# Kernel tuning notes

Hardware: AMD Instinct MI355X
Metric: run time of the kernel (lower is better)

The kernel has to match this reference:

```python
import jax, jax.numpy as jnp
import numpy as np

L, V, P, D, H, F = 6, 50257, 1024, 1024, 16, 4096
DH = D // H
EPS = 1e-5


def setup_inputs() -> dict:
    key = jax.random.key(0)
    ks = jax.random.split(key, 8)
    s = 0.02  # init scale to keep activations sane across layers
    inp = {
        "input_ids": jax.random.randint(ks[0], (2, 1024), 0, V),
        "wte": jax.random.normal(ks[1], (V, D), jnp.float32) * s,
        "wpe": jax.random.normal(ks[2], (P, D), jnp.float32) * s,
        "ln1_g": jnp.ones((L, D), jnp.float32),
        "ln1_b": jnp.zeros((L, D), jnp.float32),
        "wq": jax.random.normal(ks[3], (L, D, D), jnp.float32) * s,
        "bq": jnp.zeros((L, D), jnp.float32),
        "wk": jax.random.normal(ks[4], (L, D, D), jnp.float32) * s,
        "bk": jnp.zeros((L, D), jnp.float32),
        "wv": jax.random.normal(ks[5], (L, D, D), jnp.float32) * s,
        "bv": jnp.zeros((L, D), jnp.float32),
        "wo": jax.random.normal(jax.random.fold_in(key, 10), (L, D, D), jnp.float32) * s,
        "bo": jnp.zeros((L, D), jnp.float32),
        "ln2_g": jnp.ones((L, D), jnp.float32),
        "ln2_b": jnp.zeros((L, D), jnp.float32),
        "w1": jax.random.normal(ks[6], (L, D, F), jnp.float32) * s,
        "b1": jnp.zeros((L, F), jnp.float32),
        "w2": jax.random.normal(ks[7], (L, F, D), jnp.float32) * s,
        "b2": jnp.zeros((L, D), jnp.float32),
        "lnf_g": jnp.ones((D,), jnp.float32),
        "lnf_b": jnp.zeros((D,), jnp.float32),
    }
    return inp


def _ln(x, g, b):
    m = jnp.mean(x, axis=-1, keepdims=True)
    v = jnp.mean(jnp.square(x - m), axis=-1, keepdims=True)
    return (x - m) * jax.lax.rsqrt(v + EPS) * g + b


def _block(x, p):
    (g1, be1, wq, bq, wk, bk, wv, bv, wo, bo, g2, be2, w1, b1, w2, b2) = p
    B, T, _ = x.shape
    h = _ln(x, g1, be1)
    q = (h @ wq + bq).reshape(B, T, H, DH)
    k = (h @ wk + bk).reshape(B, T, H, DH)
    v = (h @ wv + bv).reshape(B, T, H, DH)
    scores = jnp.einsum("bqhd,bkhd->bhqk", q, k) * (1.0 / np.sqrt(DH))
    attn = jax.nn.softmax(scores, axis=-1)  # NOTE: no causal mask (as in source)
    o = jnp.einsum("bhqk,bkhd->bqhd", attn, v).reshape(B, T, D)
    x = x + o @ wo + bo
    h2 = _ln(x, g2, be2)
    x = x + jax.nn.gelu(h2 @ w1 + b1, approximate=False) @ w2 + b2
    return x


def reference(input_ids, wte, wpe, ln1_g, ln1_b, wq, bq, wk, bk, wv, bv,
              wo, bo, ln2_g, ln2_b, w1, b1, w2, b2, lnf_g, lnf_b):
    T = input_ids.shape[1]
    x = wte[input_ids] + wpe[:T]  # [B,T,D]
    params = (ln1_g, ln1_b, wq, bq, wk, bk, wv, bv, wo, bo,
              ln2_g, ln2_b, w1, b1, w2, b2)

    def step(x, p):
        return _block(x, p), None

    x, _ = jax.lax.scan(step, x, params)
    return _ln(x, lnf_g, lnf_b)
```

## Files before the change

### kernel.cpp

```cpp
#include <hip/hip_runtime.h>
#include <hip/hip_bf16.h>
#include <math.h>

#define DV 1024
#define FF 4096
#define NLAY 6
#define NH 16
#define TT 1024
#define NTOK 2048

typedef float f32x4 __attribute__((ext_vector_type(4)));
typedef short bf16x8 __attribute__((ext_vector_type(8)));
typedef unsigned short u16;
typedef u16 u16x4 __attribute__((ext_vector_type(4)));
typedef u16 u16x8 __attribute__((ext_vector_type(8)));

__device__ __forceinline__ u16 f2b(float f) {
  unsigned u = __float_as_uint(f);
  unsigned r = (u + 0x7fffu + ((u >> 16) & 1u)) >> 16;
  return (u16)r;
}
__device__ __forceinline__ float b2f(u16 u) {
  return __uint_as_float(((unsigned)u) << 16);
}

__device__ __forceinline__ void gload_lds16(const void* g, void* lds) {
  __builtin_amdgcn_global_load_lds(
      (const __attribute__((address_space(1))) void*)g,
      (__attribute__((address_space(3))) void*)lds, 16, 0, 0);
}

__global__ __launch_bounds__(256) void embed_ln_k(const int* __restrict__ ids,
                                                  const float* __restrict__ wte,
                                                  const float* __restrict__ wpe,
                                                  const float* __restrict__ gg,
                                                  const float* __restrict__ bb,
                                                  float* __restrict__ X,
                                                  u16* __restrict__ outb) {
  int row = blockIdx.x, tid = threadIdx.x;
  int t = row & (TT - 1);
  int id = ids[row];
  f32x4 a = *(const f32x4*)(wte + (size_t)id * DV + tid * 4);
  f32x4 p = *(const f32x4*)(wpe + (size_t)t * DV + tid * 4);
  f32x4 v = a + p;
  *(f32x4*)(X + (size_t)row * DV + tid * 4) = v;
  float s1 = v[0] + v[1] + v[2] + v[3];
  float s2 = v[0] * v[0] + v[1] * v[1] + v[2] * v[2] + v[3] * v[3];
#pragma unroll
  for (int o = 32; o >= 1; o >>= 1) {
    s1 += __shfl_xor(s1, o);
    s2 += __shfl_xor(s2, o);
  }
  __shared__ float sh[8];
  int w = tid >> 6;
  if ((tid & 63) == 0) { sh[w] = s1; sh[w + 4] = s2; }
  __syncthreads();
  s1 = sh[0] + sh[1] + sh[2] + sh[3];
  s2 = sh[4] + sh[5] + sh[6] + sh[7];
  float mean = s1 * (1.0f / DV);
  float var = s2 * (1.0f / DV) - mean * mean;
  float rstd = rsqrtf(var + 1e-5f);
  f32x4 gv = *(const f32x4*)(gg + tid * 4);
  f32x4 bv = *(const f32x4*)(bb + tid * 4);
  u16x4 r;
#pragma unroll
  for (int i = 0; i < 4; ++i) r[i] = f2b((v[i] - mean) * rstd * gv[i] + bv[i]);
  *(u16x4*)(outb + (size_t)row * DV + tid * 4) = r;
}

template <int OUTF>
__global__ __launch_bounds__(256) void ln_k(const float* __restrict__ X,
                                            const float* __restrict__ gg,
                                            const float* __restrict__ bb,
                                            u16* __restrict__ outb,
                                            float* __restrict__ outf) {
  int row = blockIdx.x, tid = threadIdx.x;
  f32x4 v = *(const f32x4*)(X + (size_t)row * DV + tid * 4);
  float s1 = v[0] + v[1] + v[2] + v[3];
  float s2 = v[0] * v[0] + v[1] * v[1] + v[2] * v[2] + v[3] * v[3];
#pragma unroll
  for (int o = 32; o >= 1; o >>= 1) {
    s1 += __shfl_xor(s1, o);
    s2 += __shfl_xor(s2, o);
  }
  __shared__ float sh[8];
  int w = tid >> 6;
  if ((tid & 63) == 0) { sh[w] = s1; sh[w + 4] = s2; }
  __syncthreads();
  s1 = sh[0] + sh[1] + sh[2] + sh[3];
  s2 = sh[4] + sh[5] + sh[6] + sh[7];
  float mean = s1 * (1.0f / DV);
  float var = s2 * (1.0f / DV) - mean * mean;
  float rstd = rsqrtf(var + 1e-5f);
  f32x4 gv = *(const f32x4*)(gg + tid * 4);
  f32x4 bv = *(const f32x4*)(bb + tid * 4);
  f32x4 o;
#pragma unroll
  for (int i = 0; i < 4; ++i) o[i] = (v[i] - mean) * rstd * gv[i] + bv[i];
  if (OUTF) {
    *(f32x4*)(outf + (size_t)row * DV + tid * 4) = o;
  } else {
    u16x4 r = {f2b(o[0]), f2b(o[1]), f2b(o[2]), f2b(o[3])};
    *(u16x4*)(outb + (size_t)row * DV + tid * 4) = r;
  }
}

template <int NS, int OUTF>
__global__ __launch_bounds__(256) void reduce_ln_k(
    float* __restrict__ X, const u16* __restrict__ pp,
    const float* __restrict__ bias, const float* __restrict__ gg,
    const float* __restrict__ bb, u16* __restrict__ outb,
    float* __restrict__ outf) {
  int row = blockIdx.x, tid = threadIdx.x;
  size_t off = (size_t)row * DV + tid * 4;
  f32x4 v = *(const f32x4*)(X + off);
  if (NS > 0) {
    f32x4 bvv = *(const f32x4*)(bias + tid * 4);
    v += bvv;
#pragma unroll
    for (int s = 0; s < NS; ++s) {
      u16x4 pv = *(const u16x4*)(pp + (size_t)s * NTOK * DV + off);
      v[0] += b2f(pv[0]); v[1] += b2f(pv[1]);
      v[2] += b2f(pv[2]); v[3] += b2f(pv[3]);
    }
    *(f32x4*)(X + off) = v;
  }
  float s1 = v[0] + v[1] + v[2] + v[3];
  float s2 = v[0] * v[0] + v[1] * v[1] + v[2] * v[2] + v[3] * v[3];
#pragma unroll
  for (int o = 32; o >= 1; o >>= 1) {
    s1 += __shfl_xor(s1, o);
    s2 += __shfl_xor(s2, o);
  }
  __shared__ float sh[8];
  int w = tid >> 6;
  if ((tid & 63) == 0) { sh[w] = s1; sh[w + 4] = s2; }
  __syncthreads();
  s1 = sh[0] + sh[1] + sh[2] + sh[3];
  s2 = sh[4] + sh[5] + sh[6] + sh[7];
  float mean = s1 * (1.0f / DV);
  float var = s2 * (1.0f / DV) - mean * mean;
  float rstd = rsqrtf(var + 1e-5f);
  f32x4 gv = *(const f32x4*)(gg + tid * 4);
  f32x4 bv = *(const f32x4*)(bb + tid * 4);
  f32x4 o;
#pragma unroll
  for (int i = 0; i < 4; ++i) o[i] = (v[i] - mean) * rstd * gv[i] + bv[i];
  if (OUTF) {
    *(f32x4*)(outf + off) = o;
  } else {
    u16x4 r = {f2b(o[0]), f2b(o[1]), f2b(o[2]), f2b(o[3])};
    *(u16x4*)(outb + off) = r;
  }
}

__global__ __launch_bounds__(256) void transw_k(const float* __restrict__ wq,
                                                const float* __restrict__ wk,
                                                const float* __restrict__ wv,
                                                const float* __restrict__ wo,
                                                const float* __restrict__ w1,
                                                const float* __restrict__ w2,
                                                u16* __restrict__ WT) {
  int lay = blockIdx.y;
  size_t oDD = (size_t)lay * DV * DV, oDF = (size_t)lay * DV * FF;
  u16* WTL = WT + (size_t)lay * 12 * 1024 * 1024;
  int bid = blockIdx.x;
  const float* src;
  u16* dst;
  int K, N, tile;
  if (bid < 256) {
    int which = bid >> 6;
    src = (which == 0 ? wq : which == 1 ? wk : which == 2 ? wv : wo) + oDD;
    dst = WTL + (size_t)which * (DV * DV);
    K = DV; N = DV; tile = bid & 63;
  } else if (bid < 512) {
    src = w1 + oDF; dst = WTL + (size_t)4 * (DV * DV); K = DV; N = FF; tile = bid - 256;
  } else {
    src = w2 + oDF; dst = WTL + (size_t)8 * (DV * DV); K = FF; N = DV; tile = bid - 512;
  }
  int ntc = N >> 7;
  int tr = tile / ntc, tc = tile - tr * ntc;
  int k0 = tr * 128, n0 = tc * 128;
  __shared__ u16 ts[128][130];
  int tid = threadIdx.x;
  int lr = tid >> 5, lc = (tid & 31) * 4;
#pragma unroll
  for (int p = 0; p < 16; ++p) {
    int k = p * 8 + lr;
    f32x4 v = *(const f32x4*)(src + (size_t)(k0 + k) * N + n0 + lc);
    ts[k][lc + 0] = f2b(v[0]);
    ts[k][lc + 1] = f2b(v[1]);
    ts[k][lc + 2] = f2b(v[2]);
    ts[k][lc + 3] = f2b(v[3]);
  }
  __syncthreads();
  int m = tid & 15, wn2 = tid >> 4;
#pragma unroll
  for (int p = 0; p < 8; ++p) {
    int n = p * 16 + wn2;
#pragma unroll
    for (int p2 = 0; p2 < 2; ++p2) {
      int kk = p2 * 64 + m * 4;
      u16x4 ov = {ts[kk][n], ts[kk + 1][n], ts[kk + 2][n], ts[kk + 3][n]};
      *(u16x4*)(dst + (size_t)(n0 + n) * K + k0 + kk) = ov;
    }
  }
}

template <int EPI>
__global__ __launch_bounds__(256) void gemm_k(
    const u16* __restrict__ A, const u16* __restrict__ Wt,
    const float* __restrict__ b0, const float* __restrict__ b1,
    const float* __restrict__ b2, u16* __restrict__ o0, u16* __restrict__ o1,
    u16* __restrict__ o2t, u16* __restrict__ op, float* __restrict__ of,
    const float* __restrict__ res, int M, int N, int K, int KS) {
  int z = blockIdx.z;
  const u16* W = Wt;
  const float* bias = b0;
  u16* outb = o0;
  if (EPI == 0) {
    W = Wt + (size_t)z * N * K;
    bias = z == 0 ? b0 : z == 1 ? b1 : b2;
    outb = z == 0 ? o0 : o1;
  }
  int kbeg = (EPI == 3) ? z * KS : 0;
  int klen = (EPI == 3) ? KS : K;
  int bm = blockIdx.x * 128, bn = blockIdx.y * 128;
  __shared__ __attribute__((aligned(16))) u16 As[2][128 * 64];
  __shared__ __attribute__((aligned(16))) u16 Bs[2][128 * 64];
  int tid = threadIdx.x, l = tid & 63, w = tid >> 6;
  int q = l & 15, g = l >> 4;
  int wm = (w >> 1) * 64, wn = (w & 1) * 64;
  int srow = w * 32 + (l >> 3);
  int scol = (((l & 7) ^ ((l >> 3) & 7))) * 8;
  const u16* Ab = A + (size_t)(bm + srow) * K + kbeg + scol;
  const u16* Wb = W + (size_t)(bn + srow) * K + kbeg + scol;
  f32x4 acc[4][4] = {};
  int nk = klen >> 6;
#pragma unroll
  for (int i = 0; i < 4; ++i) {
    gload_lds16(Ab + (size_t)i * 8 * K, &As[0][(w * 32 + i * 8) * 64]);
    gload_lds16(Wb + (size_t)i * 8 * K, &Bs[0][(w * 32 + i * 8) * 64]);
  }
  __syncthreads();
  for (int t = 0; t < nk; ++t) {
    int cur = t & 1;
    if (t + 1 < nk) {
      int ko = (t + 1) * 64;
#pragma unroll
      for (int i = 0; i < 4; ++i) {
        gload_lds16(Ab + (size_t)i * 8 * K + ko, &As[cur ^ 1][(w * 32 + i * 8) * 64]);
        gload_lds16(Wb + (size_t)i * 8 * K + ko, &Bs[cur ^ 1][(w * 32 + i * 8) * 64]);
      }
    }
#pragma unroll
    for (int kk = 0; kk < 2; ++kk) {
      bf16x8 af[4], bfr[4];
#pragma unroll
      for (int f = 0; f < 4; ++f) {
        int ra = wm + f * 16 + q, rb = wn + f * 16 + q;
        af[f]  = *(const bf16x8*)(&As[cur][ra * 64 + ((kk * 4 + g) ^ (ra & 7)) * 8]);
        bfr[f] = *(const bf16x8*)(&Bs[cur][rb * 64 + ((kk * 4 + g) ^ (rb & 7)) * 8]);
      }
#pragma unroll
      for (int fm = 0; fm < 4; ++fm)
#pragma unroll
        for (int fn = 0; fn < 4; ++fn)
          acc[fm][fn] = __builtin_amdgcn_mfma_f32_16x16x32_bf16(af[fm], bfr[fn],
                                                                acc[fm][fn], 0, 0, 0);
    }
    __syncthreads();
  }
#pragma unroll
  for (int fm = 0; fm < 4; ++fm) {
#pragma unroll
    for (int fn = 0; fn < 4; ++fn) {
      int gcol = bn + wn + fn * 16 + q;
      int growb = bm + wm + fm * 16 + g * 4;
      if (EPI == 3) {
        u16* pf = op + (size_t)z * M * N;
#pragma unroll
        for (int r = 0; r < 4; ++r)
          pf[(size_t)(growb + r) * N + gcol] = f2b(acc[fm][fn][r]);
      } else if (EPI == 0 && z == 2) {
        float bv = bias[gcol];
        u16x4 pv = {f2b(acc[fm][fn][0] + bv), f2b(acc[fm][fn][1] + bv),
                    f2b(acc[fm][fn][2] + bv), f2b(acc[fm][fn][3] + bv)};
        *(u16x4*)(o2t + (size_t)gcol * M + growb) = pv;
      } else {
        float bv = bias[gcol];
#pragma unroll
        for (int r = 0; r < 4; ++r) {
          float v = acc[fm][fn][r] + bv;
          if (EPI == 1) v = 0.5f * v * (1.0f + erff(v * 0.70710678118f));
          if (EPI == 2) {
            of[(size_t)(growb + r) * N + gcol] = res[(size_t)(growb + r) * N + gcol] + v;
          } else {
            outb[(size_t)(growb + r) * N + gcol] = f2b(v);
          }
        }
      }
    }
  }
}

__global__ __launch_bounds__(256) void attn_k(const u16* __restrict__ Q,
                                              const u16* __restrict__ Kb,
                                              const u16* __restrict__ Vt,
                                              u16* __restrict__ O) {
  int bid = blockIdx.x;
  int qt = bid & 15, h = (bid >> 4) & 15, b = bid >> 8;
  int tid = threadIdx.x, l = tid & 63, w = tid >> 6;
  int q = l & 15, g = l >> 4;
  int tokbase = b * TT;
  int qbase = tokbase + qt * 64 + w * 16;
  __shared__ __attribute__((aligned(16))) u16 Ks[2][32 * 64];
  __shared__ __attribute__((aligned(16))) u16 Vs[2][64 * 32];
  __shared__ __attribute__((aligned(16))) u16 Ps[4][512];
  bf16x8 qf[2];
  {
    int qrow = qbase + q;
#pragma unroll
    for (int half = 0; half < 2; ++half)
      qf[half] = *(const bf16x8*)(Q + (size_t)qrow * DV + h * 64 + half * 32 + g * 8);
  }
  int key_s = w * 8 + (l >> 3), c_s = l & 7;
  const u16* ksrc = Kb + (size_t)(tokbase + key_s) * DV + h * 64 + ((c_s ^ (key_s & 7)) * 8);
  int dl = w * 16 + (l >> 2), c2 = l & 3;
  const u16* vsrc = Vt + (size_t)(h * 64 + dl) * NTOK + tokbase + ((c2 ^ (dl & 3)) * 8);
  f32x4 oacc[4] = {};
  float m_run = -INFINITY, l_run = 0.0f;
  gload_lds16(ksrc, &Ks[0][w * 512]);
  gload_lds16(vsrc, &Vs[0][w * 512]);
  __syncthreads();
  for (int kbk = 0; kbk < TT / 32; ++kbk) {
    int cur = kbk & 1;
    if (kbk + 1 < TT / 32) {
      gload_lds16(ksrc + (size_t)(kbk + 1) * 32 * DV, &Ks[cur ^ 1][w * 512]);
      gload_lds16(vsrc + (kbk + 1) * 32, &Vs[cur ^ 1][w * 512]);
    }
    f32x4 s[2] = {};
#pragma unroll
    for (int kt = 0; kt < 2; ++kt)
#pragma unroll
      for (int half = 0; half < 2; ++half) {
        int row = kt * 16 + q;
        int chunk = (half * 4 + g) ^ (row & 7);
        bf16x8 kf = *(const bf16x8*)(&Ks[cur][row * 64 + chunk * 8]);
        s[kt] = __builtin_amdgcn_mfma_f32_16x16x32_bf16(kf, qf[half], s[kt], 0, 0, 0);
      }
    float tmax = -INFINITY;
#pragma unroll
    for (int kt = 0; kt < 2; ++kt)
#pragma unroll
      for (int r = 0; r < 4; ++r) {
        s[kt][r] *= 0.125f;
        tmax = fmaxf(tmax, s[kt][r]);
      }
    tmax = fmaxf(tmax, __shfl_xor(tmax, 16));
    tmax = fmaxf(tmax, __shfl_xor(tmax, 32));
    float m_new = fmaxf(m_run, tmax);
    float corr = __expf(m_run - m_new);
    float psum = 0.0f;
    u16 pb[2][4];
#pragma unroll
    for (int kt = 0; kt < 2; ++kt)
#pragma unroll
      for (int r = 0; r < 4; ++r) {
        float p = __expf(s[kt][r] - m_new);
        psum += p;
        pb[kt][r] = f2b(p);
      }
    psum += __shfl_xor(psum, 16);
    psum += __shfl_xor(psum, 32);
    l_run = l_run * corr + psum;
    m_run = m_new;
#pragma unroll
    for (int kt = 0; kt < 2; ++kt) {
      u16x4 pv4 = {pb[kt][0], pb[kt][1], pb[kt][2], pb[kt][3]};
      *(u16x4*)(&Ps[w][q * 32 + ((kt * 4 + g) ^ (q & 7)) * 4]) = pv4;
    }
    float corr4[4];
#pragma unroll
    for (int r = 0; r < 4; ++r) corr4[r] = __shfl(corr, g * 4 + r);
#pragma unroll
    for (int nt = 0; nt < 4; ++nt)
#pragma unroll
      for (int r = 0; r < 4; ++r) oacc[nt][r] *= corr4[r];
    u16x4 a0 = *(const u16x4*)(&Ps[w][q * 32 + ((2 * g) ^ (q & 7)) * 4]);
    u16x4 a1 = *(const u16x4*)(&Ps[w][q * 32 + ((2 * g + 1) ^ (q & 7)) * 4]);
    bf16x8 pa = {(short)a0[0], (short)a0[1], (short)a0[2], (short)a0[3],
                 (short)a1[0], (short)a1[1], (short)a1[2], (short)a1[3]};
#pragma unroll
    for (int nt = 0; nt < 4; ++nt) {
      int vrow = nt * 16 + q;
      int vc = g ^ (vrow & 3);
      bf16x8 vf = *(const bf16x8*)(&Vs[cur][vrow * 32 + vc * 8]);
      oacc[nt] = __builtin_amdgcn_mfma_f32_16x16x32_bf16(pa, vf, oacc[nt], 0, 0, 0);
    }
    __syncthreads();
  }
  float rl[4];
#pragma unroll
  for (int r = 0; r < 4; ++r) rl[r] = 1.0f / __shfl(l_run, g * 4 + r);
#pragma unroll
  for (int nt = 0; nt < 4; ++nt)
#pragma unroll
    for (int r = 0; r < 4; ++r) {
      int qrw = qbase + g * 4 + r;
      int d = nt * 16 + q;
      O[(size_t)qrw * DV + h * 64 + d] = f2b(oacc[nt][r] * rl[r]);
    }
}

extern "C" void kernel_launch(void* const* d_in, const int* in_sizes, int n_in,
                              void* d_out, int out_size, void* d_ws, size_t ws_size,
                              hipStream_t stream) {
  const int*   ids = (const int*)d_in[0];
  const float* wte = (const float*)d_in[1];
  const float* wpe = (const float*)d_in[2];
  const float* l1g = (const float*)d_in[3];
  const float* l1b = (const float*)d_in[4];
  const float* wq  = (const float*)d_in[5];
  const float* bq  = (const float*)d_in[6];
  const float* wk  = (const float*)d_in[7];
  const float* bk  = (const float*)d_in[8];
  const float* wv  = (const float*)d_in[9];
  const float* bv  = (const float*)d_in[10];
  const float* wo  = (const float*)d_in[11];
  const float* bo  = (const float*)d_in[12];
  const float* l2g = (const float*)d_in[13];
  const float* l2b = (const float*)d_in[14];
  const float* w1  = (const float*)d_in[15];
  const float* b1  = (const float*)d_in[16];
  const float* w2  = (const float*)d_in[17];
  const float* b2  = (const float*)d_in[18];
  const float* lfg = (const float*)d_in[19];
  const float* lfb = (const float*)d_in[20];
  (void)in_sizes; (void)n_in; (void)out_size;

  bool bigws = ws_size >= ((size_t)221 << 20);
  bool midws = ws_size >= ((size_t)101 << 20);

  char* ws = (char*)d_ws;
  float* x   = (float*)(ws + 0);
  u16*   hb  = (u16*)(ws + ((size_t)8 << 20));
  u16*   qb  = (u16*)(ws + ((size_t)12 << 20));
  u16*   kb  = (u16*)(ws + ((size_t)16 << 20));
  u16*   vbt = (u16*)(ws + ((size_t)20 << 20));
  u16*   ab  = (u16*)(ws + ((size_t)24 << 20));
  u16*   mb  = (u16*)(ws + ((size_t)28 << 20));
  u16*   pp  = (u16*)(ws + ((size_t)44 << 20));
  u16*   WT  = (u16*)(ws + ((size_t)(midws ? 76 : 44) << 20));

  if (bigws)
    transw_k<<<dim3(768, 6), 256, 0, stream>>>(wq, wk, wv, wo, w1, w2, WT);
  embed_ln_k<<<NTOK, 256, 0, stream>>>(ids, wte, wpe, l1g, l1b, x, hb);

  for (int lay = 0; lay < NLAY; ++lay) {
    size_t oDD = (size_t)lay * DV * DV;
    size_t oDF = (size_t)lay * DV * FF;
    u16* WTL = bigws ? WT + (size_t)lay * 12 * 1024 * 1024 : WT;
    if (!bigws)
      transw_k<<<dim3(768, 1), 256, 0, stream>>>(wq + oDD, wk + oDD, wv + oDD,
                                                 wo + oDD, w1 + oDF, w2 + oDF, WTL);
    gemm_k<0><<<dim3(16, 8, 3), 256, 0, stream>>>(
        hb, WTL, bq + lay * DV, bk + lay * DV, bv + lay * DV,
        qb, kb, vbt, nullptr, nullptr, nullptr, NTOK, DV, DV, 0);
    attn_k<<<512, 256, 0, stream>>>(qb, kb, vbt, ab);
    if (midws) {
      gemm_k<3><<<dim3(16, 8, 4), 256, 0, stream>>>(
          ab, WTL + (size_t)3 * DV * DV, nullptr, nullptr, nullptr,
          nullptr, nullptr, nullptr, pp, nullptr, nullptr, NTOK, DV, DV, 256);
      reduce_ln_k<4, 0><<<NTOK, 256, 0, stream>>>(
          x, pp, bo + lay * DV, l2g + lay * DV, l2b + lay * DV, hb, nullptr);
    } else {
      gemm_k<2><<<dim3(16, 8, 1), 256, 0, stream>>>(
          ab, WTL + (size_t)3 * DV * DV, bo + lay * DV, nullptr, nullptr,
          nullptr, nullptr, nullptr, nullptr, x, x, NTOK, DV, DV, 0);
      ln_k<0><<<NTOK, 256, 0, stream>>>(x, l2g + lay * DV, l2b + lay * DV, hb, nullptr);
    }
    gemm_k<1><<<dim3(16, 32, 1), 256, 0, stream>>>(
        hb, WTL + (size_t)4 * DV * DV, b1 + lay * FF, nullptr, nullptr,
        mb, nullptr, nullptr, nullptr, nullptr, nullptr, NTOK, FF, DV, 0);
    if (midws) {
      gemm_k<3><<<dim3(16, 8, 4), 256, 0, stream>>>(
          mb, WTL + (size_t)8 * DV * DV, nullptr, nullptr, nullptr,
          nullptr, nullptr, nullptr, pp, nullptr, nullptr, NTOK, DV, FF, 1024);
      if (lay < NLAY - 1)
        reduce_ln_k<4, 0><<<NTOK, 256, 0, stream>>>(
            x, pp, b2 + lay * DV, l1g + (lay + 1) * DV, l1b + (lay + 1) * DV,
            hb, nullptr);
      else
        reduce_ln_k<4, 1><<<NTOK, 256, 0, stream>>>(
            x, pp, b2 + lay * DV, lfg, lfb, nullptr, (float*)d_out);
    } else {
      gemm_k<2><<<dim3(16, 8, 1), 256, 0, stream>>>(
          mb, WTL + (size_t)8 * DV * DV, b2 + lay * DV, nullptr, nullptr,
          nullptr, nullptr, nullptr, nullptr, x, x, NTOK, DV, FF, 0);
      if (lay < NLAY - 1)
        ln_k<0><<<NTOK, 256, 0, stream>>>(x, l1g + (lay + 1) * DV,
                                          l1b + (lay + 1) * DV, hb, nullptr);
      else
        ln_k<1><<<NTOK, 256, 0, stream>>>(x, lfg, lfb, nullptr, (float*)d_out);
    }
  }
}
```

Measured before the change: 996.0 us.

## Triple-buffer GEMM K-loop with BK=32 and vmcnt-based waits

```diff
diff --git a/kernel.cpp b/kernel.cpp
--- a/kernel.cpp
+++ b/kernel.cpp
@@ -184,14 +184,17 @@
   __shared__ u16 ts[128][130];
   int tid = threadIdx.x;
   int lr = tid >> 5, lc = (tid & 31) * 4;
+  f32x4 vv[16];
+#pragma unroll
+  for (int p = 0; p < 16; ++p)
+    vv[p] = *(const f32x4*)(src + (size_t)(k0 + p * 8 + lr) * N + n0 + lc);
 #pragma unroll
   for (int p = 0; p < 16; ++p) {
     int k = p * 8 + lr;
-    f32x4 v = *(const f32x4*)(src + (size_t)(k0 + k) * N + n0 + lc);
-    ts[k][lc + 0] = f2b(v[0]);
-    ts[k][lc + 1] = f2b(v[1]);
-    ts[k][lc + 2] = f2b(v[2]);
-    ts[k][lc + 3] = f2b(v[3]);
+    ts[k][lc + 0] = f2b(vv[p][0]);
+    ts[k][lc + 1] = f2b(vv[p][1]);
+    ts[k][lc + 2] = f2b(vv[p][2]);
+    ts[k][lc + 3] = f2b(vv[p][3]);
   }
   __syncthreads();
   int m = tid & 15, wn2 = tid >> 4;
@@ -226,51 +229,54 @@
   int kbeg = (EPI == 3) ? z * KS : 0;
   int klen = (EPI == 3) ? KS : K;
   int bm = blockIdx.x * 128, bn = blockIdx.y * 128;
-  __shared__ __attribute__((aligned(16))) u16 As[2][128 * 64];
-  __shared__ __attribute__((aligned(16))) u16 Bs[2][128 * 64];
+  __shared__ __attribute__((aligned(16))) u16 As[3][128 * 32];
+  __shared__ __attribute__((aligned(16))) u16 Bs[3][128 * 32];
   int tid = threadIdx.x, l = tid & 63, w = tid >> 6;
   int q = l & 15, g = l >> 4;
   int wm = (w >> 1) * 64, wn = (w & 1) * 64;
-  int srow = w * 32 + (l >> 3);
-  int scol = (((l & 7) ^ ((l >> 3) & 7))) * 8;
-  const u16* Ab = A + (size_t)(bm + srow) * K + kbeg + scol;
-  const u16* Wb = W + (size_t)(bn + srow) * K + kbeg + scol;
+  const u16* Asrc = A + (size_t)(bm + (tid >> 2)) * K + kbeg + (tid & 3) * 8;
+  const u16* Wsrc = W + (size_t)(bn + (tid >> 2)) * K + kbeg + (tid & 3) * 8;
+  size_t rstep = (size_t)64 * K;
   f32x4 acc[4][4] = {};
-  int nk = klen >> 6;
-#pragma unroll
-  for (int i = 0; i < 4; ++i) {
-    gload_lds16(Ab + (size_t)i * 8 * K, &As[0][(w * 32 + i * 8) * 64]);
-    gload_lds16(Wb + (size_t)i * 8 * K, &Bs[0][(w * 32 + i * 8) * 64]);
-  }
-  __syncthreads();
+  int nk = klen >> 5;
+#define STG(b, t)                                              \
+  {                                                            \
+    int ko = (t) * 32;                                         \
+    gload_lds16(Asrc + ko, &As[b][tid * 8]);                   \
+    gload_lds16(Asrc + rstep + ko, &As[b][(tid + 256) * 8]);   \
+    gload_lds16(Wsrc + ko, &Bs[b][tid * 8]);                   \
+    gload_lds16(Wsrc + rstep + ko, &Bs[b][(tid + 256) * 8]);   \
+  }
+  STG(0, 0);
+  STG(1, 1);
   for (int t = 0; t < nk; ++t) {
-    int cur = t & 1;
-    if (t + 1 < nk) {
-      int ko = (t + 1) * 64;
-#pragma unroll
-      for (int i = 0; i < 4; ++i) {
-        gload_lds16(Ab + (size_t)i * 8 * K + ko, &As[cur ^ 1][(w * 32 + i * 8) * 64]);
-        gload_lds16(Wb + (size_t)i * 8 * K + ko, &Bs[cur ^ 1][(w * 32 + i * 8) * 64]);
-      }
-    }
-#pragma unroll
-    for (int kk = 0; kk < 2; ++kk) {
-      bf16x8 af[4], bfr[4];
-#pragma unroll
-      for (int f = 0; f < 4; ++f) {
-        int ra = wm + f * 16 + q, rb = wn + f * 16 + q;
-        af[f]  = *(const bf16x8*)(&As[cur][ra * 64 + ((kk * 4 + g) ^ (ra & 7)) * 8]);
-        bfr[f] = *(const bf16x8*)(&Bs[cur][rb * 64 + ((kk * 4 + g) ^ (rb & 7)) * 8]);
-      }
-#pragma unroll
-      for (int fm = 0; fm < 4; ++fm)
-#pragma unroll
-        for (int fn = 0; fn < 4; ++fn)
-          acc[fm][fn] = __builtin_amdgcn_mfma_f32_16x16x32_bf16(af[fm], bfr[fn],
-                                                                acc[fm][fn], 0, 0, 0);
-    }
-    __syncthreads();
-  }
+    __builtin_amdgcn_sched_barrier(0);
+    if (t + 2 < nk) {
+      asm volatile("s_waitcnt vmcnt(4)" ::: "memory");
+    } else {
+      asm volatile("s_waitcnt vmcnt(0)" ::: "memory");
+    }
+    __builtin_amdgcn_s_barrier();
+    __builtin_amdgcn_sched_barrier(0);
+    if (t + 2 < nk) {
+      int b2i = (t + 2) % 3;
+      STG(b2i, t + 2);
+    }
+    int cur = t % 3;
+    bf16x8 af[4], bfr[4];
+#pragma unroll
+    for (int f = 0; f < 4; ++f) {
+      af[f]  = *(const bf16x8*)(&As[cur][(wm + f * 16 + q) * 32 + g * 8]);
+      bfr[f] = *(const bf16x8*)(&Bs[cur][(wn + f * 16 + q) * 32 + g * 8]);
+    }
+#pragma unroll
+    for (int fm = 0; fm < 4; ++fm)
+#pragma unroll
+      for (int fn = 0; fn < 4; ++fn)
+        acc[fm][fn] = __builtin_amdgcn_mfma_f32_16x16x32_bf16(af[fm], bfr[fn],
+                                                              acc[fm][fn], 0, 0, 0);
+  }
+#undef STG
 #pragma unroll
   for (int fm = 0; fm < 4; ++fm) {
 #pragma unroll
```

Measured after the change: 1.109 ms. 11.3% more time.

## Stage GEMM epilogue through LDS for vectorized stores; split V projection; retune split-K

Applied to the files above, without the earlier changes.

```diff
diff --git a/kernel.cpp b/kernel.cpp
--- a/kernel.cpp
+++ b/kernel.cpp
@@ -164,7 +164,8 @@
   int lay = blockIdx.y;
   size_t oDD = (size_t)lay * DV * DV, oDF = (size_t)lay * DV * FF;
   u16* WTL = WT + (size_t)lay * 12 * 1024 * 1024;
-  int bid = blockIdx.x;
+  int b0 = blockIdx.x;
+  int bid = (b0 & 7) * 96 + (b0 >> 3);
   const float* src;
   u16* dst;
   int K, N, tile;
@@ -184,23 +185,26 @@
   __shared__ u16 ts[128][130];
   int tid = threadIdx.x;
   int lr = tid >> 5, lc = (tid & 31) * 4;
+  f32x4 vv[16];
+#pragma unroll
+  for (int p = 0; p < 16; ++p)
+    vv[p] = *(const f32x4*)(src + (size_t)(k0 + p * 8 + lr) * N + n0 + lc);
 #pragma unroll
   for (int p = 0; p < 16; ++p) {
     int k = p * 8 + lr;
-    f32x4 v = *(const f32x4*)(src + (size_t)(k0 + k) * N + n0 + lc);
-    ts[k][lc + 0] = f2b(v[0]);
-    ts[k][lc + 1] = f2b(v[1]);
-    ts[k][lc + 2] = f2b(v[2]);
-    ts[k][lc + 3] = f2b(v[3]);
-  }
-  __syncthreads();
-  int m = tid & 15, wn2 = tid >> 4;
+    ts[k][lc + 0] = f2b(vv[p][0]);
+    ts[k][lc + 1] = f2b(vv[p][1]);
+    ts[k][lc + 2] = f2b(vv[p][2]);
+    ts[k][lc + 3] = f2b(vv[p][3]);
+  }
+  __syncthreads();
+  int m = tid & 15, u2 = tid >> 4;
 #pragma unroll
   for (int p = 0; p < 8; ++p) {
-    int n = p * 16 + wn2;
-#pragma unroll
-    for (int p2 = 0; p2 < 2; ++p2) {
-      int kk = p2 * 64 + m * 4;
+    int n = p * 16 + u2;
+#pragma unroll
+    for (int s = 0; s < 2; ++s) {
+      int kk = s * 64 + m * 4;
       u16x4 ov = {ts[kk][n], ts[kk + 1][n], ts[kk + 2][n], ts[kk + 3][n]};
       *(u16x4*)(dst + (size_t)(n0 + n) * K + k0 + kk) = ov;
     }
@@ -211,7 +215,7 @@
 __global__ __launch_bounds__(256) void gemm_k(
     const u16* __restrict__ A, const u16* __restrict__ Wt,
     const float* __restrict__ b0, const float* __restrict__ b1,
-    const float* __restrict__ b2, u16* __restrict__ o0, u16* __restrict__ o1,
+    u16* __restrict__ o0, u16* __restrict__ o1,
     u16* __restrict__ o2t, u16* __restrict__ op, float* __restrict__ of,
     const float* __restrict__ res, int M, int N, int K, int KS) {
   int z = blockIdx.z;
@@ -220,14 +224,16 @@
   u16* outb = o0;
   if (EPI == 0) {
     W = Wt + (size_t)z * N * K;
-    bias = z == 0 ? b0 : z == 1 ? b1 : b2;
+    bias = z == 0 ? b0 : b1;
     outb = z == 0 ? o0 : o1;
   }
   int kbeg = (EPI == 3) ? z * KS : 0;
   int klen = (EPI == 3) ? KS : K;
   int bm = blockIdx.x * 128, bn = blockIdx.y * 128;
-  __shared__ __attribute__((aligned(16))) u16 As[2][128 * 64];
-  __shared__ __attribute__((aligned(16))) u16 Bs[2][128 * 64];
+  __shared__ __attribute__((aligned(16))) u16 SM[32768];
+  u16* As = SM;
+  u16* Bs = SM + 16384;
+  u16* Cs = SM;
   int tid = threadIdx.x, l = tid & 63, w = tid >> 6;
   int q = l & 15, g = l >> 4;
   int wm = (w >> 1) * 64, wn = (w & 1) * 64;
@@ -239,8 +245,8 @@
   int nk = klen >> 6;
 #pragma unroll
   for (int i = 0; i < 4; ++i) {
-    gload_lds16(Ab + (size_t)i * 8 * K, &As[0][(w * 32 + i * 8) * 64]);
-    gload_lds16(Wb + (size_t)i * 8 * K, &Bs[0][(w * 32 + i * 8) * 64]);
+    gload_lds16(Ab + (size_t)i * 8 * K, &As[(w * 32 + i * 8) * 64]);
+    gload_lds16(Wb + (size_t)i * 8 * K, &Bs[(w * 32 + i * 8) * 64]);
   }
   __syncthreads();
   for (int t = 0; t < nk; ++t) {
@@ -249,8 +255,10 @@
       int ko = (t + 1) * 64;
 #pragma unroll
       for (int i = 0; i < 4; ++i) {
-        gload_lds16(Ab + (size_t)i * 8 * K + ko, &As[cur ^ 1][(w * 32 + i * 8) * 64]);
-        gload_lds16(Wb + (size_t)i * 8 * K + ko, &Bs[cur ^ 1][(w * 32 + i * 8) * 64]);
+        gload_lds16(Ab + (size_t)i * 8 * K + ko,
+                    &As[(cur ^ 1) * 8192 + (w * 32 + i * 8) * 64]);
+        gload_lds16(Wb + (size_t)i * 8 * K + ko,
+                    &Bs[(cur ^ 1) * 8192 + (w * 32 + i * 8) * 64]);
       }
     }
 #pragma unroll
@@ -259,8 +267,8 @@
 #pragma unroll
       for (int f = 0; f < 4; ++f) {
         int ra = wm + f * 16 + q, rb = wn + f * 16 + q;
-        af[f]  = *(const bf16x8*)(&As[cur][ra * 64 + ((kk * 4 + g) ^ (ra & 7)) * 8]);
-        bfr[f] = *(const bf16x8*)(&Bs[cur][rb * 64 + ((kk * 4 + g) ^ (rb & 7)) * 8]);
+        af[f]  = *(const bf16x8*)(&As[cur * 8192 + ra * 64 + ((kk * 4 + g) ^ (ra & 7)) * 8]);
+        bfr[f] = *(const bf16x8*)(&Bs[cur * 8192 + rb * 64 + ((kk * 4 + g) ^ (rb & 7)) * 8]);
       }
 #pragma unroll
       for (int fm = 0; fm < 4; ++fm)
@@ -271,34 +279,52 @@
     }
     __syncthreads();
   }
+  if (EPI == 2) {
+#pragma unroll
+    for (int fm = 0; fm < 4; ++fm)
+#pragma unroll
+      for (int fn = 0; fn < 4; ++fn) {
+        int gcol = bn + wn + fn * 16 + q;
+        int growb = bm + wm + fm * 16 + g * 4;
+        float bv = bias[gcol];
+#pragma unroll
+        for (int r = 0; r < 4; ++r)
+          of[(size_t)(growb + r) * N + gcol] = res[(size_t)(growb + r) * N + gcol]
+                                               + acc[fm][fn][r] + bv;
+      }
+    return;
+  }
 #pragma unroll
   for (int fm = 0; fm < 4; ++fm) {
 #pragma unroll
     for (int fn = 0; fn < 4; ++fn) {
-      int gcol = bn + wn + fn * 16 + q;
-      int growb = bm + wm + fm * 16 + g * 4;
-      if (EPI == 3) {
-        u16* pf = op + (size_t)z * M * N;
-#pragma unroll
-        for (int r = 0; r < 4; ++r)
-          pf[(size_t)(growb + r) * N + gcol] = f2b(acc[fm][fn][r]);
-      } else if (EPI == 0 && z == 2) {
-        float bv = bias[gcol];
-        u16x4 pv = {f2b(acc[fm][fn][0] + bv), f2b(acc[fm][fn][1] + bv),
-                    f2b(acc[fm][fn][2] + bv), f2b(acc[fm][fn][3] + bv)};
-        *(u16x4*)(o2t + (size_t)gcol * M + growb) = pv;
+      int cL = wn + fn * 16 + q;
+      float bv = (EPI == 3) ? 0.0f : bias[bn + cL];
+#pragma unroll
+      for (int r = 0; r < 4; ++r) {
+        int rL = wm + fm * 16 + g * 4 + r;
+        float v = acc[fm][fn][r] + bv;
+        if (EPI == 1) v = 0.5f * v * (1.0f + erff(v * 0.70710678118f));
+        if (EPI == 4) Cs[cL * 132 + rL] = f2b(v);
+        else          Cs[rL * 132 + cL] = f2b(v);
+      }
+    }
+  }
+  __syncthreads();
+  {
+    int rowL = tid >> 4, c8 = (tid & 15) * 8;
+#pragma unroll
+    for (int p = 0; p < 8; ++p) {
+      int row = p * 16 + rowL;
+      u16x4 lo = *(const u16x4*)(&Cs[row * 132 + c8]);
+      u16x4 hi = *(const u16x4*)(&Cs[row * 132 + c8 + 4]);
+      u16x8 ov = {lo[0], lo[1], lo[2], lo[3], hi[0], hi[1], hi[2], hi[3]};
+      if (EPI == 4) {
+        *(u16x8*)(o2t + (size_t)(bn + row) * M + bm + c8) = ov;
+      } else if (EPI == 3) {
+        *(u16x8*)(op + (size_t)z * M * N + (size_t)(bm + row) * N + bn + c8) = ov;
       } else {
-        float bv = bias[gcol];
-#pragma unroll
-        for (int r = 0; r < 4; ++r) {
-          float v = acc[fm][fn][r] + bv;
-          if (EPI == 1) v = 0.5f * v * (1.0f + erff(v * 0.70710678118f));
-          if (EPI == 2) {
-            of[(size_t)(growb + r) * N + gcol] = res[(size_t)(growb + r) * N + gcol] + v;
-          } else {
-            outb[(size_t)(growb + r) * N + gcol] = f2b(v);
-          }
-        }
+        *(u16x8*)(outb + (size_t)(bm + row) * N + bn + c8) = ov;
       }
     }
   }
@@ -464,28 +490,31 @@
     if (!bigws)
       transw_k<<<dim3(768, 1), 256, 0, stream>>>(wq + oDD, wk + oDD, wv + oDD,
                                                  wo + oDD, w1 + oDF, w2 + oDF, WTL);
-    gemm_k<0><<<dim3(16, 8, 3), 256, 0, stream>>>(
-        hb, WTL, bq + lay * DV, bk + lay * DV, bv + lay * DV,
-        qb, kb, vbt, nullptr, nullptr, nullptr, NTOK, DV, DV, 0);
+    gemm_k<0><<<dim3(16, 8, 2), 256, 0, stream>>>(
+        hb, WTL, bq + lay * DV, bk + lay * DV,
+        qb, kb, nullptr, nullptr, nullptr, nullptr, NTOK, DV, DV, 0);
+    gemm_k<4><<<dim3(16, 8, 1), 256, 0, stream>>>(
+        hb, WTL + (size_t)2 * DV * DV, bv + lay * DV, nullptr,
+        nullptr, nullptr, vbt, nullptr, nullptr, nullptr, NTOK, DV, DV, 0);
     attn_k<<<512, 256, 0, stream>>>(qb, kb, vbt, ab);
     if (midws) {
-      gemm_k<3><<<dim3(16, 8, 4), 256, 0, stream>>>(
-          ab, WTL + (size_t)3 * DV * DV, nullptr, nullptr, nullptr,
-          nullptr, nullptr, nullptr, pp, nullptr, nullptr, NTOK, DV, DV, 256);
-      reduce_ln_k<4, 0><<<NTOK, 256, 0, stream>>>(
+      gemm_k<3><<<dim3(16, 8, 2), 256, 0, stream>>>(
+          ab, WTL + (size_t)3 * DV * DV, nullptr, nullptr,
+          nullptr, nullptr, nullptr, pp, nullptr, nullptr, NTOK, DV, DV, 512);
+      reduce_ln_k<2, 0><<<NTOK, 256, 0, stream>>>(
           x, pp, bo + lay * DV, l2g + lay * DV, l2b + lay * DV, hb, nullptr);
     } else {
       gemm_k<2><<<dim3(16, 8, 1), 256, 0, stream>>>(
-          ab, WTL + (size_t)3 * DV * DV, bo + lay * DV, nullptr, nullptr,
+          ab, WTL + (size_t)3 * DV * DV, bo + lay * DV, nullptr,
           nullptr, nullptr, nullptr, nullptr, x, x, NTOK, DV, DV, 0);
       ln_k<0><<<NTOK, 256, 0, stream>>>(x, l2g + lay * DV, l2b + lay * DV, hb, nullptr);
     }
     gemm_k<1><<<dim3(16, 32, 1), 256, 0, stream>>>(
-        hb, WTL + (size_t)4 * DV * DV, b1 + lay * FF, nullptr, nullptr,
+        hb, WTL + (size_t)4 * DV * DV, b1 + lay * FF, nullptr,
         mb, nullptr, nullptr, nullptr, nullptr, nullptr, NTOK, FF, DV, 0);
     if (midws) {
       gemm_k<3><<<dim3(16, 8, 4), 256, 0, stream>>>(
-          mb, WTL + (size_t)8 * DV * DV, nullptr, nullptr, nullptr,
+          mb, WTL + (size_t)8 * DV * DV, nullptr, nullptr,
           nullptr, nullptr, nullptr, pp, nullptr, nullptr, NTOK, DV, FF, 1024);
       if (lay < NLAY - 1)
         reduce_ln_k<4, 0><<<NTOK, 256, 0, stream>>>(
@@ -496,7 +525,7 @@
             x, pp, b2 + lay * DV, lfg, lfb, nullptr, (float*)d_out);
     } else {
       gemm_k<2><<<dim3(16, 8, 1), 256, 0, stream>>>(
-          mb, WTL + (size_t)8 * DV * DV, b2 + lay * DV, nullptr, nullptr,
+          mb, WTL + (size_t)8 * DV * DV, b2 + lay * DV, nullptr,
           nullptr, nullptr, nullptr, nullptr, x, x, NTOK, DV, FF, 0);
       if (lay < NLAY - 1)
         ln_k<0><<<NTOK, 256, 0, stream>>>(x, l1g + (lay + 1) * DV,
```

Result: no change. 1.007 ms (+1.1%).
